# Optimization experiments

Measured on AMD Instinct MI355X. Metric: run time of the kernel, lower is better.

The kernel has to match this reference:

```python
import jax, jax.numpy as jnp
import numpy as np

B, T, D, H, K = 8, 1024, 512, 8, 33
DK = D // H
PAD = (K - 1) // 2
EPS = 1e-5


def _ln(x, g, b):
    m = x.mean(-1, keepdims=True)
    v = ((x - m) ** 2).mean(-1, keepdims=True)
    return (x - m) / jnp.sqrt(v + EPS) * g + b


def _ffn(x, g, b, w1, b1, w2, b2):
    h = jax.nn.silu(_ln(x, g, b) @ w1 + b1)
    return h @ w2 + b2


def _rel_shift(x):
    # x: [B, H, T1, T2]
    b, h, t1, t2 = x.shape
    x = jnp.pad(x, ((0, 0), (0, 0), (0, 0), (1, 0)))
    x = x.reshape(b, h, t2 + 1, t1)[:, :, 1:, :].reshape(b, h, t1, t2)
    return x[..., :t1]


def setup_inputs() -> dict:
    key = jax.random.key(0)
    ks = iter(jax.random.split(key, 40))
    rn = lambda *s: jax.random.normal(next(ks), s, jnp.float32) * 0.02
    inp = {
        'x': jax.random.normal(next(ks), (B, T, D), jnp.float32),
        'pos_emb': jax.random.normal(next(ks), (1, T, D), jnp.float32),
        # ffn1
        'ln1_g': jnp.ones((D,), jnp.float32), 'ln1_b': jnp.zeros((D,), jnp.float32),
        'ffn1_w1': rn(D, 4 * D), 'ffn1_b1': jnp.zeros((4 * D,), jnp.float32),
        'ffn1_w2': rn(4 * D, D), 'ffn1_b2': jnp.zeros((D,), jnp.float32),
        # mhsa
        'lnq_g': jnp.ones((D,), jnp.float32), 'lnq_b': jnp.zeros((D,), jnp.float32),
        'lnk_g': jnp.ones((D,), jnp.float32), 'lnk_b': jnp.zeros((D,), jnp.float32),
        'lnv_g': jnp.ones((D,), jnp.float32), 'lnv_b': jnp.zeros((D,), jnp.float32),
        'wq': rn(D, D), 'wk': rn(D, D), 'wv': rn(D, D), 'wpos': rn(D, D),
        'pos_bias_u': jnp.zeros((H, DK), jnp.float32),
        'pos_bias_v': jnp.zeros((H, DK), jnp.float32),
        'wfc': rn(D, D),
        # conv module
        'cln_g': jnp.ones((D,), jnp.float32), 'cln_b': jnp.zeros((D,), jnp.float32),
        'pw1': rn(D, 4 * D),             # pointwise_conv1 weight as [in, out]
        'dw_w': rn(2 * D, 1, K),         # depthwise conv weight [C, 1, K]
        'bn_g': jnp.ones((2 * D,), jnp.float32), 'bn_b': jnp.zeros((2 * D,), jnp.float32),
        'pw2': rn(2 * D, D),
        # ffn2
        'ln2_g': jnp.ones((D,), jnp.float32), 'ln2_b': jnp.zeros((D,), jnp.float32),
        'ffn2_w1': rn(D, 4 * D), 'ffn2_b1': jnp.zeros((4 * D,), jnp.float32),
        'ffn2_w2': rn(4 * D, D), 'ffn2_b2': jnp.zeros((D,), jnp.float32),
        # final layer norm
        'lnf_g': jnp.ones((D,), jnp.float32), 'lnf_b': jnp.zeros((D,), jnp.float32),
    }
    return inp


def reference(x, pos_emb, ln1_g, ln1_b, ffn1_w1, ffn1_b1, ffn1_w2, ffn1_b2,
              lnq_g, lnq_b, lnk_g, lnk_b, lnv_g, lnv_b, wq, wk, wv, wpos,
              pos_bias_u, pos_bias_v, wfc,
              cln_g, cln_b, pw1, dw_w, bn_g, bn_b, pw2,
              ln2_g, ln2_b, ffn2_w1, ffn2_b1, ffn2_w2, ffn2_b2, lnf_g, lnf_b):
    b, t, d = x.shape
    scale = 1.0 / DK ** 0.5

    # ---- FFN1 (half-step) ----
    out = 0.5 * x + 0.5 * (x + _ffn(x, ln1_g, ln1_b, ffn1_w1, ffn1_b1, ffn1_w2, ffn1_b2))

    # ---- rel-pos MHSA ----
    res = out
    q = (_ln(out, lnq_g, lnq_b) @ wq).reshape(b, t, H, DK)            # [B,T,H,dk]
    k = (_ln(out, lnk_g, lnk_b) @ wk).reshape(b, t, H, DK).transpose(0, 2, 1, 3)
    v = (_ln(out, lnv_g, lnv_b) @ wv).reshape(b, t, H, DK).transpose(0, 2, 1, 3)
    p = (pos_emb @ wpos).reshape(pos_emb.shape[0], -1, H, DK).transpose(0, 2, 3, 1)  # [1,H,dk,Tp]

    q_u = (q + pos_bias_u).transpose(0, 2, 1, 3)                      # [B,H,T,dk]
    q_v = (q + pos_bias_v).transpose(0, 2, 1, 3)
    matrix_bd = _rel_shift(jnp.matmul(q_v, p) * scale)                # [B,H,T,T]
    scores = jnp.einsum('bhqd,bhkd->bhqk', q_u, k) * scale + matrix_bd
    attn = jax.nn.softmax(scores, axis=-1)
    o = jnp.einsum('bhqk,bhkd->bhqd', attn, v)
    out = o.transpose(0, 2, 1, 3).reshape(b, t, d) @ wfc + res

    # ---- convolution module ----
    res = out
    h = _ln(out, cln_g, cln_b) @ pw1                                  # [B,T,4D]
    a, g = jnp.split(h, 2, axis=-1)
    h = a * jax.nn.sigmoid(g)                                         # GLU -> [B,T,2D]
    h = jax.lax.conv_general_dilated(
        h.transpose(0, 2, 1), dw_w, window_strides=(1,),
        padding=[(PAD, PAD)], feature_group_count=2 * D,
        dimension_numbers=('NCH', 'OIH', 'NCH')).transpose(0, 2, 1)
    h = jax.nn.silu(_ln(h, bn_g, bn_b))
    out = h @ pw2 + res

    # ---- FFN2 (half-step) + final LN ----
    out = 0.5 * out + 0.5 * (out + _ffn(out, ln2_g, ln2_b, ffn2_w1, ffn2_b1, ffn2_w2, ffn2_b2))
    return _ln(out, lnf_g, lnf_b)
```

## Files before the change

kernel.cpp:

```cpp
#include <hip/hip_runtime.h>

typedef unsigned short bf16u;
typedef __attribute__((ext_vector_type(8))) short bf16x8;
typedef __attribute__((ext_vector_type(4))) float f32x4;

__device__ __forceinline__ float bf2f(bf16u u) {
    return __uint_as_float(((unsigned)u) << 16);
}
__device__ __forceinline__ bf16u f2bf(float f) {
    unsigned u = __float_as_uint(f);
    unsigned r = (u + 0x7fffu + ((u >> 16) & 1u)) >> 16;
    return (bf16u)r;
}
__device__ __forceinline__ float sigmoidf_(float x) {
    return 1.0f / (1.0f + __expf(-x));
}

__device__ __forceinline__ void gload_lds16(const bf16u* g, bf16u* l) {
    __builtin_amdgcn_global_load_lds(
        (const __attribute__((address_space(1))) unsigned int*)(const void*)g,
        (__attribute__((address_space(3))) unsigned int*)(void*)l, 16, 0, 0);
}

__global__ void init_flag_kernel(int* flag) {
    if (threadIdx.x == 0 && blockIdx.x == 0) *flag = 0;
}
__global__ __launch_bounds__(256) void detect_kernel(
    const void* x, int nelem, int* flag)
{
    const int scan = nelem < (1 << 20) ? nelem : (1 << 20);
    const bf16u* p = (const bf16u*)x;
    int bad = 0;
    for (int j = blockIdx.x * 256 + threadIdx.x; j < scan; j += 65536) {
        unsigned u = p[j];
        if ((u & 0x7F80u) == 0x7F80u) bad = 1;
    }
    if (bad) atomicOr(flag, 1);
}

__global__ __launch_bounds__(256) void cvt_bf_kernel(
    const void* __restrict__ in, bf16u* __restrict__ out, int n,
    const int* __restrict__ flagp)
{
    const int f32 = *flagp;
    const int i = blockIdx.x * 256 + threadIdx.x;
    if (i >= n) return;
    if (f32) out[i] = f2bf(((const float*)in)[i]);
    else     out[i] = ((const bf16u*)in)[i];
}

__global__ __launch_bounds__(256) void wtrans_kernel(
    const void* __restrict__ W, bf16u* __restrict__ Wt, int K, int N,
    const int* __restrict__ flagp)
{
    __shared__ float tile[32][33];
    const int f32 = *flagp;
    const int n0 = blockIdx.x * 32, k0 = blockIdx.y * 32;
    const int tx = threadIdx.x & 31, ty = threadIdx.x >> 5;
    #pragma unroll
    for (int r = 0; r < 4; ++r) {
        const int k = ty + r * 8;
        float v;
        if (f32) v = ((const float*)W)[(size_t)(k0 + k) * N + n0 + tx];
        else     v = bf2f(((const bf16u*)W)[(size_t)(k0 + k) * N + n0 + tx]);
        tile[k][tx] = v;
    }
    __syncthreads();
    #pragma unroll
    for (int r = 0; r < 4; ++r) {
        const int n = ty + r * 8;
        Wt[(size_t)(n0 + n) * K + k0 + tx] = f2bf(tile[tx][n]);
    }
}

__global__ __launch_bounds__(256) void vtrans_kernel(
    const bf16u* __restrict__ vb, bf16u* __restrict__ vt)
{
    __shared__ bf16u tile[32][33];
    const int j0 = blockIdx.x * 32;
    const int h = blockIdx.y >> 1, dt = (blockIdx.y & 1) * 32;
    const int b = blockIdx.z;
    const int tx = threadIdx.x & 31, ty = threadIdx.x >> 5;
    #pragma unroll
    for (int r = 0; r < 4; ++r) {
        const int j = ty + r * 8;
        tile[j][tx] = vb[(size_t)(b * 1024 + j0 + j) * 512 + h * 64 + dt + tx];
    }
    __syncthreads();
    #pragma unroll
    for (int r = 0; r < 4; ++r) {
        const int d = ty + r * 8;
        vt[(size_t)((b * 8 + h) * 64 + dt + d) * 1024 + j0 + tx] = tile[tx][d];
    }
}

__global__ __launch_bounds__(256) void add_qbias_kernel(
    const bf16u* __restrict__ qb, const void* __restrict__ bu,
    const void* __restrict__ bv, bf16u* __restrict__ qu,
    bf16u* __restrict__ qv, const int* __restrict__ flagp)
{
    const int f32 = *flagp;
    const int idx = blockIdx.x * 256 + threadIdx.x;
    const int c = idx & 511;
    const float q = bf2f(qb[idx]);
    float ub, vbias;
    if (f32) { ub = ((const float*)bu)[c]; vbias = ((const float*)bv)[c]; }
    else     { ub = bf2f(((const bf16u*)bu)[c]); vbias = bf2f(((const bf16u*)bv)[c]); }
    qu[idx] = f2bf(q + ub);
    qv[idx] = f2bf(q + vbias);
}

template <int D, int IN_MODE, int OUT_MODE, bool SILU, bool COPY>
__global__ __launch_bounds__(256) void ln_kernel(
    const void* __restrict__ in_, const void* __restrict__ gvec,
    const void* __restrict__ bvec, void* __restrict__ out_,
    float* __restrict__ copy_out, const int* __restrict__ flagp)
{
    constexpr int VPT = D / 256;
    const int f32 = *flagp;
    const int row = blockIdx.x;
    const int tid = threadIdx.x;
    const size_t base = (size_t)row * D;
    float x[VPT];
    if (IN_MODE == 2 || (IN_MODE == 1 && !f32)) {
        const bf16u* in = (const bf16u*)in_;
        #pragma unroll
        for (int i = 0; i < VPT; ++i) x[i] = bf2f(in[base + tid + i * 256]);
    } else {
        const float* in = (const float*)in_;
        #pragma unroll
        for (int i = 0; i < VPT; ++i) x[i] = in[base + tid + i * 256];
    }
    float s = 0.f, q = 0.f;
    #pragma unroll
    for (int i = 0; i < VPT; ++i) { s += x[i]; q += x[i] * x[i]; }
    __shared__ float red[10];
    #pragma unroll
    for (int off = 32; off; off >>= 1) {
        s += __shfl_down(s, off, 64);
        q += __shfl_down(q, off, 64);
    }
    const int lane = tid & 63, wv = tid >> 6;
    if (lane == 0) { red[wv] = s; red[4 + wv] = q; }
    __syncthreads();
    if (tid == 0) {
        float ts = red[0] + red[1] + red[2] + red[3];
        float tq = red[4] + red[5] + red[6] + red[7];
        float mean = ts / (float)D;
        float var = tq / (float)D - mean * mean;
        red[8] = mean;
        red[9] = rsqrtf(var + 1e-5f);
    }
    __syncthreads();
    const float mean = red[8], rstd = red[9];
    #pragma unroll
    for (int i = 0; i < VPT; ++i) {
        const int c = tid + i * 256;
        float gv, bv;
        if (f32) {
            gv = ((const float*)gvec)[c];
            bv = ((const float*)bvec)[c];
        } else {
            gv = bf2f(((const bf16u*)gvec)[c]);
            bv = bf2f(((const bf16u*)bvec)[c]);
        }
        float v = (x[i] - mean) * rstd * gv + bv;
        if (SILU) v *= sigmoidf_(v);
        if (OUT_MODE == 0) {
            ((bf16u*)out_)[base + c] = f2bf(v);
        } else {
            if (f32) ((float*)out_)[base + c] = v;
            else     ((bf16u*)out_)[base + c] = f2bf(v);
        }
        if (COPY) copy_out[base + c] = x[i];
    }
}

template <int TM>
__global__ __launch_bounds__(256) void gemm_mfma(
    const bf16u* __restrict__ A, const bf16u* __restrict__ Wt,
    const void* __restrict__ bias, const float* __restrict__ res,
    void* __restrict__ C, int M, int N, int K, float alpha, int act,
    int outbf, const int* __restrict__ flagp)
{
    constexpr int CHUNKS_A = TM * 4;
    constexpr int TOT = CHUNKS_A + 512;
    constexpr int CPW = TOT / 4;
    constexpr int ISSUES = CPW / 64;
    constexpr int BUFSZ = (TM + 128) * 32;
    constexpr int MI = 4;
    constexpr int NJ = (TM == 128) ? 4 : 2;
    __shared__ bf16u sh[2 * BUFSZ];
    const int f32 = *flagp;
    const int tid = threadIdx.x;
    const int bm = blockIdx.y * TM, bn = blockIdx.x * 128;
    const int lane = tid & 63, wvid = tid >> 6;
    const int wm = (TM == 128) ? (wvid >> 1) * 64 : 0;
    const int wn = (TM == 128) ? (wvid & 1) * 64 : wvid * 32;

    f32x4 acc[MI][NJ];
    {
        f32x4 z = {0.f, 0.f, 0.f, 0.f};
        #pragma unroll
        for (int i = 0; i < MI; ++i)
            #pragma unroll
            for (int j = 0; j < NJ; ++j) acc[i][j] = z;
    }
    const int kq = (lane >> 4) * 8, fr = lane & 15;

    #define STAGE_G(k0, bsel)                                                   \
    {                                                                           \
        bf16u* base_ = sh + (bsel) * BUFSZ;                                     \
        _Pragma("unroll")                                                       \
        for (int t = 0; t < ISSUES; ++t) {                                      \
            const int cc = wvid * CPW + t * 64 + lane;                          \
            const bf16u* src_;                                                  \
            if (cc < CHUNKS_A)                                                  \
                src_ = A + (size_t)(bm + (cc >> 2)) * K + (k0) + (cc & 3) * 8;  \
            else {                                                              \
                const int cb_ = cc - CHUNKS_A;                                  \
                src_ = Wt + (size_t)(bn + (cb_ >> 2)) * K + (k0) + (cb_ & 3) * 8;\
            }                                                                   \
            gload_lds16(src_, base_ + (wvid * CPW + t * 64) * 8);               \
        }                                                                       \
    }

    const int KT = K / 32;
    STAGE_G(0, 0);
    for (int kt = 0; kt < KT; ++kt) {
        __syncthreads();
        if (kt + 1 < KT) STAGE_G((kt + 1) * 32, (kt + 1) & 1);
        const bf16u* buf = sh + (kt & 1) * BUFSZ;
        bf16x8 af[MI], bfr[NJ];
        #pragma unroll
        for (int i = 0; i < MI; ++i)
            af[i] = *(const bf16x8*)&buf[(wm + i * 16 + fr) * 32 + kq];
        #pragma unroll
        for (int j = 0; j < NJ; ++j)
            bfr[j] = *(const bf16x8*)&buf[TM * 32 + (wn + j * 16 + fr) * 32 + kq];
        #pragma unroll
        for (int i = 0; i < MI; ++i)
            #pragma unroll
            for (int j = 0; j < NJ; ++j)
                acc[i][j] = __builtin_amdgcn_mfma_f32_16x16x32_bf16(
                    af[i], bfr[j], acc[i][j], 0, 0, 0);
    }
    #undef STAGE_G

    const int quad = lane >> 4, col = lane & 15;
    #pragma unroll
    for (int j = 0; j < NJ; ++j) {
        const int n = bn + wn + j * 16 + col;
        float bv = 0.f;
        if (bias) bv = f32 ? ((const float*)bias)[n]
                           : bf2f(((const bf16u*)bias)[n]);
        #pragma unroll
        for (int i = 0; i < MI; ++i) {
            #pragma unroll
            for (int r = 0; r < 4; ++r) {
                const int m = bm + wm + i * 16 + quad * 4 + r;
                float v = acc[i][j][r] + bv;
                if (act == 1) v *= sigmoidf_(v);
                v *= alpha;
                const size_t off = (size_t)m * N + n;
                if (res) v += res[off];
                if (outbf) ((bf16u*)C)[off] = f2bf(v);
                else       ((float*)C)[off] = v;
            }
        }
    }
}

__global__ __launch_bounds__(256) void attn_score_mfma(
    const bf16u* __restrict__ qu, const bf16u* __restrict__ qv,
    const bf16u* __restrict__ kb, const bf16u* __restrict__ pb,
    bf16u* __restrict__ S, bf16u* __restrict__ BD)
{
    constexpr int BUFSZ = 8192;
    __shared__ bf16u sh[2 * BUFSZ];
    const int tid = threadIdx.x;
    const int z = blockIdx.z;
    const int h = z & 7, which = z >> 3;
    const bf16u* A = which ? qv : qu;
    const bf16u* B = which ? pb : kb;
    bf16u* C = (which ? BD : S) + (size_t)h * 1048576;
    const int hoff = h * 64;
    const int bm = blockIdx.y * 128, bn = blockIdx.x * 128;
    const int lane = tid & 63, wvid = tid >> 6;
    const int wm = (wvid >> 1) * 64, wn = (wvid & 1) * 64;
    const int kq = (lane >> 4) * 8, fr = lane & 15;

    f32x4 acc[4][4];
    {
        f32x4 zr = {0.f, 0.f, 0.f, 0.f};
        #pragma unroll
        for (int i = 0; i < 4; ++i)
            #pragma unroll
            for (int j = 0; j < 4; ++j) acc[i][j] = zr;
    }

    #define STAGE_S(k0, bsel)                                                   \
    {                                                                           \
        bf16u* base_ = sh + (bsel) * BUFSZ;                                     \
        _Pragma("unroll")                                                       \
        for (int t = 0; t < 4; ++t) {                                           \
            const int cc = wvid * 256 + t * 64 + lane;                          \
            const bf16u* src_;                                                  \
            if (cc < 512)                                                       \
                src_ = A + (size_t)(bm + (cc >> 2)) * 512 + hoff + (k0) + (cc & 3) * 8; \
            else {                                                              \
                const int cb_ = cc - 512;                                       \
                src_ = B + (size_t)(bn + (cb_ >> 2)) * 512 + hoff + (k0) + (cb_ & 3) * 8; \
            }                                                                   \
            gload_lds16(src_, base_ + (wvid * 256 + t * 64) * 8);               \
        }                                                                       \
    }

    STAGE_S(0, 0);
    #pragma unroll
    for (int kt = 0; kt < 2; ++kt) {
        __syncthreads();
        if (kt == 0) STAGE_S(32, 1);
        const bf16u* buf = sh + (kt & 1) * BUFSZ;
        bf16x8 af[4], bfr[4];
        #pragma unroll
        for (int i = 0; i < 4; ++i)
            af[i] = *(const bf16x8*)&buf[(wm + i * 16 + fr) * 32 + kq];
        #pragma unroll
        for (int j = 0; j < 4; ++j)
            bfr[j] = *(const bf16x8*)&buf[4096 + (wn + j * 16 + fr) * 32 + kq];
        #pragma unroll
        for (int i = 0; i < 4; ++i)
            #pragma unroll
            for (int j = 0; j < 4; ++j)
                acc[i][j] = __builtin_amdgcn_mfma_f32_16x16x32_bf16(
                    af[i], bfr[j], acc[i][j], 0, 0, 0);
    }
    #undef STAGE_S

    const int quad = lane >> 4, col = lane & 15;
    #pragma unroll
    for (int j = 0; j < 4; ++j) {
        const int n = bn + wn + j * 16 + col;
        #pragma unroll
        for (int i = 0; i < 4; ++i) {
            #pragma unroll
            for (int r = 0; r < 4; ++r) {
                const int m = bm + wm + i * 16 + quad * 4 + r;
                C[(size_t)m * 1024 + n] = f2bf(acc[i][j][r] * 0.125f);
            }
        }
    }
}

__global__ __launch_bounds__(256) void attn_softmax_kernel(
    bf16u* __restrict__ S, const bf16u* __restrict__ BD)
{
    const int i = blockIdx.x, h = blockIdx.y;
    const int tid = threadIdx.x;
    bf16u* srow = S + (size_t)h * 1048576 + (size_t)i * 1024;
    const bf16u* bd0 = BD + (size_t)h * 1048576 + (size_t)i * 1024;
    const bf16u* bd1 = bd0 + 1024;
    float v[4];
    #pragma unroll
    for (int k = 0; k < 4; ++k) {
        const int j = tid + k * 256;
        float bd;
        if (j <= i)          bd = bf2f(bd0[1023 - i + j]);
        else if (j == i + 1) bd = 0.f;
        else                 bd = bf2f(bd1[j - i - 2]);
        v[k] = bf2f(srow[j]) + bd;
    }
    __shared__ float red[6];
    float m = fmaxf(fmaxf(v[0], v[1]), fmaxf(v[2], v[3]));
    #pragma unroll
    for (int off = 32; off; off >>= 1) m = fmaxf(m, __shfl_down(m, off, 64));
    const int lane = tid & 63, w = tid >> 6;
    if (lane == 0) red[w] = m;
    __syncthreads();
    if (tid == 0) red[4] = fmaxf(fmaxf(red[0], red[1]), fmaxf(red[2], red[3]));
    __syncthreads();
    m = red[4];
    float e[4], l = 0.f;
    #pragma unroll
    for (int k = 0; k < 4; ++k) { e[k] = __expf(v[k] - m); l += e[k]; }
    #pragma unroll
    for (int off = 32; off; off >>= 1) l += __shfl_down(l, off, 64);
    if (lane == 0) red[w] = l;
    __syncthreads();
    if (tid == 0) red[5] = red[0] + red[1] + red[2] + red[3];
    __syncthreads();
    const float inv = 1.0f / red[5];
    #pragma unroll
    for (int k = 0; k < 4; ++k) srow[tid + k * 256] = f2bf(e[k] * inv);
}

__global__ __launch_bounds__(256) void attn_pv_mfma(
    const bf16u* __restrict__ P, const bf16u* __restrict__ Vt,
    bf16u* __restrict__ O)
{
    constexpr int BUFSZ = 4096;
    __shared__ bf16u sh[2 * BUFSZ];
    const int tid = threadIdx.x;
    const int h = blockIdx.y;
    const int bm = blockIdx.x * 64;
    const int hoff = h * 64;
    const bf16u* Ph = P + (size_t)h * 1048576;
    const bf16u* Vh = Vt + (size_t)h * 65536;
    const int lane = tid & 63, wvid = tid >> 6;
    const int wm = wvid * 16;
    const int kq = (lane >> 4) * 8, fr = lane & 15;

    f32x4 acc[4];
    {
        f32x4 z = {0.f, 0.f, 0.f, 0.f};
        #pragma unroll
        for (int j = 0; j < 4; ++j) acc[j] = z;
    }

    #define STAGE_P(k0, bsel)                                                   \
    {                                                                           \
        bf16u* base_ = sh + (bsel) * BUFSZ;                                     \
        _Pragma("unroll")                                                       \
        for (int t = 0; t < 2; ++t) {                                           \
            const int cc = wvid * 128 + t * 64 + lane;                          \
            const bf16u* src_;                                                  \
            if (cc < 256)                                                       \
                src_ = Ph + (size_t)(bm + (cc >> 2)) * 1024 + (k0) + (cc & 3) * 8; \
            else {                                                              \
                const int cb_ = cc - 256;                                       \
                src_ = Vh + (size_t)(cb_ >> 2) * 1024 + (k0) + (cb_ & 3) * 8;   \
            }                                                                   \
            gload_lds16(src_, base_ + (wvid * 128 + t * 64) * 8);               \
        }                                                                       \
    }

    STAGE_P(0, 0);
    for (int kt = 0; kt < 32; ++kt) {
        __syncthreads();
        if (kt + 1 < 32) STAGE_P((kt + 1) * 32, (kt + 1) & 1);
        const bf16u* buf = sh + (kt & 1) * BUFSZ;
        bf16x8 af = *(const bf16x8*)&buf[(wm + fr) * 32 + kq];
        #pragma unroll
        for (int j = 0; j < 4; ++j) {
            bf16x8 bf = *(const bf16x8*)&buf[2048 + (j * 16 + fr) * 32 + kq];
            acc[j] = __builtin_amdgcn_mfma_f32_16x16x32_bf16(af, bf, acc[j], 0, 0, 0);
        }
    }
    #undef STAGE_P

    const int quad = lane >> 4, col = lane & 15;
    #pragma unroll
    for (int j = 0; j < 4; ++j) {
        const int d = j * 16 + col;
        #pragma unroll
        for (int r = 0; r < 4; ++r) {
            const int m = bm + wm + quad * 4 + r;
            O[(size_t)m * 512 + hoff + d] = f2bf(acc[j][r]);
        }
    }
}

__global__ __launch_bounds__(256) void glu_kernel(
    const bf16u* __restrict__ H, bf16u* __restrict__ out, int total)
{
    const int idx = blockIdx.x * 256 + threadIdx.x;
    if (idx >= total) return;
    const int m = idx >> 10, c = idx & 1023;
    const float a = bf2f(H[(size_t)m * 2048 + c]);
    const float g = bf2f(H[(size_t)m * 2048 + 1024 + c]);
    out[idx] = f2bf(a * sigmoidf_(g));
}

__global__ __launch_bounds__(256) void dwconv_kernel(
    const bf16u* __restrict__ in, const void* __restrict__ wp,
    bf16u* __restrict__ out, const int* __restrict__ flagp)
{
    const int f32 = *flagp;
    const int cb = blockIdx.x & 1;
    const int ttile = (blockIdx.x >> 1) & 127;
    const int b = blockIdx.x >> 8;
    const int t0 = ttile * 8;
    const int c = cb * 512 + threadIdx.x * 2;

    float w0[33], w1[33];
    if (f32) {
        const float* wf = (const float*)wp;
        #pragma unroll
        for (int k = 0; k < 33; ++k) { w0[k] = wf[c * 33 + k]; w1[k] = wf[(c + 1) * 33 + k]; }
    } else {
        const bf16u* wb = (const bf16u*)wp;
        #pragma unroll
        for (int k = 0; k < 33; ++k) { w0[k] = bf2f(wb[c * 33 + k]); w1[k] = bf2f(wb[(c + 1) * 33 + k]); }
    }

    unsigned win[40];
    #pragma unroll
    for (int r = 0; r < 40; ++r) {
        const int tt = t0 - 16 + r;
        win[r] = (tt >= 0 && tt < 1024)
               ? *(const unsigned*)(in + (size_t)(b * 1024 + tt) * 1024 + c)
               : 0u;
    }
    float acc0[8] = {}, acc1[8] = {};
    #pragma unroll
    for (int k = 0; k < 33; ++k) {
        #pragma unroll
        for (int dt = 0; dt < 8; ++dt) {
            const unsigned u = win[dt + k];
            acc0[dt] = fmaf(bf2f((bf16u)(u & 0xffffu)), w0[k], acc0[dt]);
            acc1[dt] = fmaf(bf2f((bf16u)(u >> 16)), w1[k], acc1[dt]);
        }
    }
    #pragma unroll
    for (int dt = 0; dt < 8; ++dt) {
        unsigned o = (unsigned)f2bf(acc0[dt]) | ((unsigned)f2bf(acc1[dt]) << 16);
        *(unsigned*)(out + (size_t)(b * 1024 + t0 + dt) * 1024 + c) = o;
    }
}

static inline void launch_gemm(const bf16u* A, const bf16u* Wt, const void* bias,
                               const float* res, void* C, int M, int N, int K,
                               float alpha, int act, int outbf, const int* flagp,
                               hipStream_t stream)
{
    if (N >= 1024) {
        dim3 grid(N / 128, M / 128);
        gemm_mfma<128><<<grid, 256, 0, stream>>>(A, Wt, bias, res, C, M, N, K, alpha, act, outbf, flagp);
    } else {
        dim3 grid(N / 128, M / 64);
        gemm_mfma<64><<<grid, 256, 0, stream>>>(A, Wt, bias, res, C, M, N, K, alpha, act, outbf, flagp);
    }
}

extern "C" void kernel_launch(void* const* d_in, const int* in_sizes, int n_in,
                              void* d_out, int out_size, void* d_ws, size_t ws_size,
                              hipStream_t stream)
{
    const void* x       = d_in[0];
    const void* pos_emb = d_in[1];
    const void* ln1_g   = d_in[2];
    const void* ln1_b   = d_in[3];
    const void* ffn1_w1 = d_in[4];
    const void* ffn1_b1 = d_in[5];
    const void* ffn1_w2 = d_in[6];
    const void* ffn1_b2 = d_in[7];
    const void* lnq_g   = d_in[8];
    const void* lnq_b   = d_in[9];
    const void* lnk_g   = d_in[10];
    const void* lnk_b   = d_in[11];
    const void* lnv_g   = d_in[12];
    const void* lnv_b   = d_in[13];
    const void* wq      = d_in[14];
    const void* wk      = d_in[15];
    const void* wv      = d_in[16];
    const void* wpos    = d_in[17];
    const void* pbu     = d_in[18];
    const void* pbv     = d_in[19];
    const void* wfc     = d_in[20];
    const void* cln_g   = d_in[21];
    const void* cln_b   = d_in[22];
    const void* pw1     = d_in[23];
    const void* dw_w    = d_in[24];
    const void* bn_g    = d_in[25];
    const void* bn_b    = d_in[26];
    const void* pw2     = d_in[27];
    const void* ln2_g   = d_in[28];
    const void* ln2_b   = d_in[29];
    const void* ffn2_w1 = d_in[30];
    const void* ffn2_b1 = d_in[31];
    const void* ffn2_w2 = d_in[32];
    const void* ffn2_b2 = d_in[33];
    const void* lnf_g   = d_in[34];
    const void* lnf_b   = d_in[35];

    const int BT = 8192;
    char* wsb = (char*)d_ws;
    float* act  = (float*)(wsb + 0);
    bf16u* qb   = (bf16u*)(wsb + 16777216);
    bf16u* kb   = (bf16u*)(wsb + 25165824);
    bf16u* vb   = (bf16u*)(wsb + 33554432);
    bf16u* pb   = (bf16u*)(wsb + 41943040);
    bf16u* tmpb = (bf16u*)(wsb + 42991616);
    bf16u* qu   = (bf16u*)(wsb + 51380224);
    bf16u* qv   = (bf16u*)(wsb + 59768832);
    bf16u* vt   = (bf16u*)(wsb + 68157440);
    bf16u* S    = (bf16u*)(wsb + 76546048);
    bf16u* BD   = (bf16u*)(wsb + 93323264);
    bf16u* wc   = (bf16u*)(wsb + 110100480);
    int* flagp  = (int*)(wsb + 124256256);
    bf16u* obb  = tmpb;
    bf16u* hbf  = (bf16u*)(wsb + 51380224);
    bf16u* Gbf  = (bf16u*)(wsb + 84934656);
    bf16u* DWbf = (bf16u*)(wsb + 16777216);
    bf16u* LObf = (bf16u*)(wsb + 33554432);

    bf16u* w_ffn1_1 = wc + 0;
    bf16u* w_ffn1_2 = wc + 1048576;
    bf16u* w_q      = wc + 2097152;
    bf16u* w_k      = wc + 2359296;
    bf16u* w_v      = wc + 2621440;
    bf16u* w_pos    = wc + 2883584;
    bf16u* w_fc     = wc + 3145728;
    bf16u* w_pw1    = wc + 3407872;
    bf16u* w_pw2    = wc + 4456448;
    bf16u* w_ffn2_1 = wc + 4980736;
    bf16u* w_ffn2_2 = wc + 6029312;

    init_flag_kernel<<<1, 64, 0, stream>>>(flagp);
    detect_kernel<<<256, 256, 0, stream>>>(x, in_sizes[0], flagp);

    wtrans_kernel<<<dim3(64, 16), 256, 0, stream>>>(ffn1_w1, w_ffn1_1, 512, 2048, flagp);
    wtrans_kernel<<<dim3(16, 64), 256, 0, stream>>>(ffn1_w2, w_ffn1_2, 2048, 512, flagp);
    wtrans_kernel<<<dim3(16, 16), 256, 0, stream>>>(wq, w_q, 512, 512, flagp);
    wtrans_kernel<<<dim3(16, 16), 256, 0, stream>>>(wk, w_k, 512, 512, flagp);
    wtrans_kernel<<<dim3(16, 16), 256, 0, stream>>>(wv, w_v, 512, 512, flagp);
    wtrans_kernel<<<dim3(16, 16), 256, 0, stream>>>(wpos, w_pos, 512, 512, flagp);
    wtrans_kernel<<<dim3(16, 16), 256, 0, stream>>>(wfc, w_fc, 512, 512, flagp);
    wtrans_kernel<<<dim3(64, 16), 256, 0, stream>>>(pw1, w_pw1, 512, 2048, flagp);
    wtrans_kernel<<<dim3(16, 32), 256, 0, stream>>>(pw2, w_pw2, 1024, 512, flagp);
    wtrans_kernel<<<dim3(64, 16), 256, 0, stream>>>(ffn2_w1, w_ffn2_1, 512, 2048, flagp);
    wtrans_kernel<<<dim3(16, 64), 256, 0, stream>>>(ffn2_w2, w_ffn2_2, 2048, 512, flagp);

    cvt_bf_kernel<<<2048, 256, 0, stream>>>(pos_emb, tmpb, 524288, flagp);
    launch_gemm(tmpb, w_pos, nullptr, nullptr, pb, 1024, 512, 512, 1.0f, 0, 1, flagp, stream);

    ln_kernel<512, 1, 0, false, true><<<BT, 256, 0, stream>>>(x, ln1_g, ln1_b, tmpb, act, flagp);
    launch_gemm(tmpb, w_ffn1_1, ffn1_b1, nullptr, hbf, BT, 2048, 512, 1.0f, 1, 1, flagp, stream);
    launch_gemm(hbf, w_ffn1_2, ffn1_b2, act, act, BT, 512, 2048, 0.5f, 0, 0, flagp, stream);

    ln_kernel<512, 0, 0, false, false><<<BT, 256, 0, stream>>>(act, lnq_g, lnq_b, tmpb, nullptr, flagp);
    launch_gemm(tmpb, w_q, nullptr, nullptr, qb, BT, 512, 512, 1.0f, 0, 1, flagp, stream);
    ln_kernel<512, 0, 0, false, false><<<BT, 256, 0, stream>>>(act, lnk_g, lnk_b, tmpb, nullptr, flagp);
    launch_gemm(tmpb, w_k, nullptr, nullptr, kb, BT, 512, 512, 1.0f, 0, 1, flagp, stream);
    ln_kernel<512, 0, 0, false, false><<<BT, 256, 0, stream>>>(act, lnv_g, lnv_b, tmpb, nullptr, flagp);
    launch_gemm(tmpb, w_v, nullptr, nullptr, vb, BT, 512, 512, 1.0f, 0, 1, flagp, stream);

    add_qbias_kernel<<<16384, 256, 0, stream>>>(qb, pbu, pbv, qu, qv, flagp);
    vtrans_kernel<<<dim3(32, 16, 8), 256, 0, stream>>>(vb, vt);

    for (int b = 0; b < 8; ++b) {
        const bf16u* qu_b = qu + (size_t)b * 524288;
        const bf16u* qv_b = qv + (size_t)b * 524288;
        const bf16u* kb_b = kb + (size_t)b * 524288;
        const bf16u* vt_b = vt + (size_t)b * 524288;
        bf16u* ob_b = obb + (size_t)b * 524288;
        attn_score_mfma<<<dim3(8, 8, 16), 256, 0, stream>>>(qu_b, qv_b, kb_b, pb, S, BD);
        attn_softmax_kernel<<<dim3(1024, 8), 256, 0, stream>>>(S, BD);
        attn_pv_mfma<<<dim3(16, 8), 256, 0, stream>>>(S, vt_b, ob_b);
    }
    launch_gemm(obb, w_fc, nullptr, act, act, BT, 512, 512, 1.0f, 0, 0, flagp, stream);

    ln_kernel<512, 0, 0, false, false><<<BT, 256, 0, stream>>>(act, cln_g, cln_b, tmpb, nullptr, flagp);
    launch_gemm(tmpb, w_pw1, nullptr, nullptr, hbf, BT, 2048, 512, 1.0f, 0, 1, flagp, stream);
    glu_kernel<<<32768, 256, 0, stream>>>(hbf, Gbf, 8388608);
    dwconv_kernel<<<2048, 256, 0, stream>>>(Gbf, dw_w, DWbf, flagp);
    ln_kernel<1024, 2, 0, true, false><<<BT, 256, 0, stream>>>(DWbf, bn_g, bn_b, LObf, nullptr, flagp);
    launch_gemm(LObf, w_pw2, nullptr, act, act, BT, 512, 1024, 1.0f, 0, 0, flagp, stream);

    ln_kernel<512, 0, 0, false, false><<<BT, 256, 0, stream>>>(act, ln2_g, ln2_b, tmpb, nullptr, flagp);
    launch_gemm(tmpb, w_ffn2_1, ffn2_b1, nullptr, hbf, BT, 2048, 512, 1.0f, 1, 1, flagp, stream);
    launch_gemm(hbf, w_ffn2_2, ffn2_b2, act, act, BT, 512, 2048, 0.5f, 0, 0, flagp, stream);

    ln_kernel<512, 0, 1, false, false><<<BT, 256, 0, stream>>>(act, lnf_g, lnf_b, d_out, nullptr, flagp);
}
```

Measured before the change: 950.9 us.

## Triple-buffer GEMM loads, remap block order, and batch attention two at a time

The GEMM and PV kernels move from double to triple buffering. The barrier now waits with a partial vmcnt, so loads for tile kt+2 stay in flight while tile kt is computed. The GEMM block index is remapped so consecutive blocks walk down M first, sharing the same weight column tile for L2 reuse. The attention loop now handles two batches per launch, which doubles grid size and halves launch count, at the cost of larger S/BD workspace buffers and more LDS per block.

```diff
diff --git a/kernel.cpp b/kernel.cpp
--- a/kernel.cpp
+++ b/kernel.cpp
@@ -190,10 +190,13 @@
     constexpr int BUFSZ = (TM + 128) * 32;
     constexpr int MI = 4;
     constexpr int NJ = (TM == 128) ? 4 : 2;
-    __shared__ bf16u sh[2 * BUFSZ];
+    __shared__ bf16u sh[3 * BUFSZ];
     const int f32 = *flagp;
     const int tid = threadIdx.x;
-    const int bm = blockIdx.y * TM, bn = blockIdx.x * 128;
+    const int mtiles = M / TM;
+    const int lid = blockIdx.y * gridDim.x + blockIdx.x;
+    const int bm = (lid % mtiles) * TM;
+    const int bn = (lid / mtiles) * 128;
     const int lane = tid & 63, wvid = tid >> 6;
     const int wm = (TM == 128) ? (wvid >> 1) * 64 : 0;
     const int wn = (TM == 128) ? (wvid & 1) * 64 : wvid * 32;
@@ -208,9 +211,9 @@
     }
     const int kq = (lane >> 4) * 8, fr = lane & 15;
 
-    #define STAGE_G(k0, bsel)                                                   \
+    #define STAGE_G(k0, bufp)                                                   \
     {                                                                           \
-        bf16u* base_ = sh + (bsel) * BUFSZ;                                     \
+        bf16u* base_ = (bufp);                                                  \
         _Pragma("unroll")                                                       \
         for (int t = 0; t < ISSUES; ++t) {                                      \
             const int cc = wvid * CPW + t * 64 + lane;                          \
@@ -226,11 +229,19 @@
     }
 
     const int KT = K / 32;
-    STAGE_G(0, 0);
+    STAGE_G(0, sh);
+    STAGE_G(32, sh + BUFSZ);
+    int bufidx = 0;
     for (int kt = 0; kt < KT; ++kt) {
-        __syncthreads();
-        if (kt + 1 < KT) STAGE_G((kt + 1) * 32, (kt + 1) & 1);
-        const bf16u* buf = sh + (kt & 1) * BUFSZ;
+        if (kt + 1 < KT)
+            asm volatile("s_waitcnt vmcnt(%0)\ns_barrier" :: "i"(ISSUES) : "memory");
+        else
+            asm volatile("s_waitcnt vmcnt(0)\ns_barrier" ::: "memory");
+        if (kt + 2 < KT) {
+            int nb = bufidx + 2; if (nb >= 3) nb -= 3;
+            STAGE_G((kt + 2) * 32, sh + nb * BUFSZ);
+        }
+        const bf16u* buf = sh + bufidx * BUFSZ;
         bf16x8 af[MI], bfr[NJ];
         #pragma unroll
         for (int i = 0; i < MI; ++i)
@@ -244,6 +255,7 @@
             for (int j = 0; j < NJ; ++j)
                 acc[i][j] = __builtin_amdgcn_mfma_f32_16x16x32_bf16(
                     af[i], bfr[j], acc[i][j], 0, 0, 0);
+        ++bufidx; if (bufidx == 3) bufidx = 0;
     }
     #undef STAGE_G
 
@@ -280,10 +292,10 @@
     __shared__ bf16u sh[2 * BUFSZ];
     const int tid = threadIdx.x;
     const int z = blockIdx.z;
-    const int h = z & 7, which = z >> 3;
-    const bf16u* A = which ? qv : qu;
-    const bf16u* B = which ? pb : kb;
-    bf16u* C = (which ? BD : S) + (size_t)h * 1048576;
+    const int h = z & 7, bb = (z >> 3) & 1, which = z >> 4;
+    const bf16u* A = (which ? qv : qu) + (size_t)bb * 524288;
+    const bf16u* B = which ? pb : (kb + (size_t)bb * 524288);
+    bf16u* C = (which ? BD : S) + (size_t)(bb * 8 + h) * 1048576;
     const int hoff = h * 64;
     const int bm = blockIdx.y * 128, bn = blockIdx.x * 128;
     const int lane = tid & 63, wvid = tid >> 6;
@@ -356,10 +368,11 @@
 __global__ __launch_bounds__(256) void attn_softmax_kernel(
     bf16u* __restrict__ S, const bf16u* __restrict__ BD)
 {
-    const int i = blockIdx.x, h = blockIdx.y;
+    const int i = blockIdx.x, h = blockIdx.y, bb = blockIdx.z;
     const int tid = threadIdx.x;
-    bf16u* srow = S + (size_t)h * 1048576 + (size_t)i * 1024;
-    const bf16u* bd0 = BD + (size_t)h * 1048576 + (size_t)i * 1024;
+    const size_t hb = (size_t)(bb * 8 + h) * 1048576;
+    bf16u* srow = S + hb + (size_t)i * 1024;
+    const bf16u* bd0 = BD + hb + (size_t)i * 1024;
     const bf16u* bd1 = bd0 + 1024;
     float v[4];
     #pragma unroll
@@ -400,13 +413,14 @@
     bf16u* __restrict__ O)
 {
     constexpr int BUFSZ = 4096;
-    __shared__ bf16u sh[2 * BUFSZ];
+    __shared__ bf16u sh[3 * BUFSZ];
     const int tid = threadIdx.x;
-    const int h = blockIdx.y;
+    const int h = blockIdx.y, bb = blockIdx.z;
     const int bm = blockIdx.x * 64;
     const int hoff = h * 64;
-    const bf16u* Ph = P + (size_t)h * 1048576;
-    const bf16u* Vh = Vt + (size_t)h * 65536;
+    const bf16u* Ph = P + (size_t)(bb * 8 + h) * 1048576;
+    const bf16u* Vh = Vt + (size_t)bb * 524288 + (size_t)h * 65536;
+    bf16u* Ob = O + (size_t)bb * 524288;
     const int lane = tid & 63, wvid = tid >> 6;
     const int wm = wvid * 16;
     const int kq = (lane >> 4) * 8, fr = lane & 15;
@@ -418,9 +432,9 @@
         for (int j = 0; j < 4; ++j) acc[j] = z;
     }
 
-    #define STAGE_P(k0, bsel)                                                   \
+    #define STAGE_P(k0, bufp)                                                   \
     {                                                                           \
-        bf16u* base_ = sh + (bsel) * BUFSZ;                                     \
+        bf16u* base_ = (bufp);                                                  \
         _Pragma("unroll")                                                       \
         for (int t = 0; t < 2; ++t) {                                           \
             const int cc = wvid * 128 + t * 64 + lane;                          \
@@ -435,17 +449,26 @@
         }                                                                       \
     }
 
-    STAGE_P(0, 0);
+    STAGE_P(0, sh);
+    STAGE_P(32, sh + BUFSZ);
+    int bufidx = 0;
     for (int kt = 0; kt < 32; ++kt) {
-        __syncthreads();
-        if (kt + 1 < 32) STAGE_P((kt + 1) * 32, (kt + 1) & 1);
-        const bf16u* buf = sh + (kt & 1) * BUFSZ;
+        if (kt + 1 < 32)
+            asm volatile("s_waitcnt vmcnt(2)\ns_barrier" ::: "memory");
+        else
+            asm volatile("s_waitcnt vmcnt(0)\ns_barrier" ::: "memory");
+        if (kt + 2 < 32) {
+            int nb = bufidx + 2; if (nb >= 3) nb -= 3;
+            STAGE_P((kt + 2) * 32, sh + nb * BUFSZ);
+        }
+        const bf16u* buf = sh + bufidx * BUFSZ;
         bf16x8 af = *(const bf16x8*)&buf[(wm + fr) * 32 + kq];
         #pragma unroll
         for (int j = 0; j < 4; ++j) {
             bf16x8 bf = *(const bf16x8*)&buf[2048 + (j * 16 + fr) * 32 + kq];
             acc[j] = __builtin_amdgcn_mfma_f32_16x16x32_bf16(af, bf, acc[j], 0, 0, 0);
         }
+        ++bufidx; if (bufidx == 3) bufidx = 0;
     }
     #undef STAGE_P
 
@@ -456,7 +479,7 @@
         #pragma unroll
         for (int r = 0; r < 4; ++r) {
             const int m = bm + wm + quad * 4 + r;
-            O[(size_t)m * 512 + hoff + d] = f2bf(acc[j][r]);
+            Ob[(size_t)m * 512 + hoff + d] = f2bf(acc[j][r]);
         }
     }
 }
@@ -586,9 +609,9 @@
     bf16u* qv   = (bf16u*)(wsb + 59768832);
     bf16u* vt   = (bf16u*)(wsb + 68157440);
     bf16u* S    = (bf16u*)(wsb + 76546048);
-    bf16u* BD   = (bf16u*)(wsb + 93323264);
-    bf16u* wc   = (bf16u*)(wsb + 110100480);
-    int* flagp  = (int*)(wsb + 124256256);
+    bf16u* BD   = (bf16u*)(wsb + 110100480);
+    bf16u* wc   = (bf16u*)(wsb + 143654912);
+    int* flagp  = (int*)(wsb + 157810688);
     bf16u* obb  = tmpb;
     bf16u* hbf  = (bf16u*)(wsb + 51380224);
     bf16u* Gbf  = (bf16u*)(wsb + 84934656);
@@ -639,15 +662,15 @@
     add_qbias_kernel<<<16384, 256, 0, stream>>>(qb, pbu, pbv, qu, qv, flagp);
     vtrans_kernel<<<dim3(32, 16, 8), 256, 0, stream>>>(vb, vt);
 
-    for (int b = 0; b < 8; ++b) {
-        const bf16u* qu_b = qu + (size_t)b * 524288;
-        const bf16u* qv_b = qv + (size_t)b * 524288;
-        const bf16u* kb_b = kb + (size_t)b * 524288;
-        const bf16u* vt_b = vt + (size_t)b * 524288;
-        bf16u* ob_b = obb + (size_t)b * 524288;
-        attn_score_mfma<<<dim3(8, 8, 16), 256, 0, stream>>>(qu_b, qv_b, kb_b, pb, S, BD);
-        attn_softmax_kernel<<<dim3(1024, 8), 256, 0, stream>>>(S, BD);
-        attn_pv_mfma<<<dim3(16, 8), 256, 0, stream>>>(S, vt_b, ob_b);
+    for (int b0 = 0; b0 < 8; b0 += 2) {
+        const bf16u* qu_b = qu + (size_t)b0 * 524288;
+        const bf16u* qv_b = qv + (size_t)b0 * 524288;
+        const bf16u* kb_b = kb + (size_t)b0 * 524288;
+        const bf16u* vt_b = vt + (size_t)b0 * 524288;
+        bf16u* ob_b = obb + (size_t)b0 * 524288;
+        attn_score_mfma<<<dim3(8, 8, 32), 256, 0, stream>>>(qu_b, qv_b, kb_b, pb, S, BD);
+        attn_softmax_kernel<<<dim3(1024, 8, 2), 256, 0, stream>>>(S, BD);
+        attn_pv_mfma<<<dim3(16, 8, 2), 256, 0, stream>>>(S, vt_b, ob_b);
     }
     launch_gemm(obb, w_fc, nullptr, act, act, BT, 512, 512, 1.0f, 0, 0, flagp, stream);
 
```

Result: faster. 835.3 us (-12.2%).
